# Optimization experiments

Hardware: AMD Instinct MI355X
Metric: run time of the kernel (lower is better)

The kernel has to match this reference:

```python
import jax, jax.numpy as jnp
import numpy as np

NEG = -1e6  # mask fill value used by d2l.sequence_mask


def setup_inputs() -> dict:
    key = jax.random.key(0)
    k1, k2, k3, k4, k5, k6, k7 = jax.random.split(key, 7)
    B, Q, K, DQ, DK, H, DV = 8, 256, 1024, 256, 256, 128, 128
    queries = jax.random.normal(k1, (B, Q, DQ), dtype=jnp.float32)
    keys = jax.random.normal(k2, (B, K, DK), dtype=jnp.float32)
    values = jax.random.normal(k3, (B, K, DV), dtype=jnp.float32)
    valid_lens = jax.random.randint(k4, (B,), 1, K + 1, dtype=jnp.int32)
    # learned params (nn.Linear stores weight as [out, in]; apply as x @ W.T)
    W_q = jax.random.normal(k5, (H, DQ), dtype=jnp.float32) / np.sqrt(DQ)
    W_k = jax.random.normal(k6, (H, DK), dtype=jnp.float32) / np.sqrt(DK)
    w_v = jax.random.normal(k7, (H,), dtype=jnp.float32) / np.sqrt(H)
    return {"queries": queries, "keys": keys, "values": values,
            "valid_lens": valid_lens, "W_q": W_q, "W_k": W_k, "w_v": w_v}


def reference(queries, keys, values, valid_lens, W_q, W_k, w_v):
    # projections
    q = jnp.einsum('bqd,hd->bqh', queries, W_q)   # [B,Q,H]
    k = jnp.einsum('bkd,hd->bkh', keys, W_k)      # [B,K,H]
    # broadcast add + tanh -> [B,Q,K,H] (the fusion-headroom intermediate)
    features = jnp.tanh(q[:, :, None, :] + k[:, None, :, :])
    scores = jnp.einsum('bqkh,h->bqk', features, w_v)  # [B,Q,K]
    # masked softmax: valid_lens is per-batch (dim==1 path)
    klen = scores.shape[-1]
    mask = jnp.arange(klen)[None, None, :] < valid_lens[:, None, None]
    scores = jnp.where(mask, scores, NEG)
    weights = jax.nn.softmax(scores, axis=-1)
    # dropout is identity in eval mode
    return jnp.einsum('bqk,bkv->bqv', weights, values)
```

## Files before the change

kernel.cpp:

```cpp
#include <hip/hip_runtime.h>


#define Bb 8
#define Qn 256
#define Kk 1024
#define Dd 256
#define Hh 128
#define DVv 128

__device__ __forceinline__ float fexp2(float x) { return __builtin_amdgcn_exp2f(x); }
__device__ __forceinline__ float frcp(float x)  { return __builtin_amdgcn_rcpf(x); }

__global__ __launch_bounds__(256)
void repack_w(const float* __restrict__ Wq, const float* __restrict__ Wk,
              float4* __restrict__ Wq4T, float4* __restrict__ Wk4T)
{
    const int blk = blockIdx.x;
    const float* src = (blk < 32) ? Wq : Wk;
    float4*      dst = (blk < 32) ? Wq4T : Wk4T;
    const int idx = (blk & 31) * 256 + threadIdx.x;
    const int g = idx >> 7;
    const int h = idx & 127;
    dst[idx] = *(const float4*)(src + (size_t)h * Dd + g * 4);
}

__global__ __launch_bounds__(512)
void proj_exp_kernel(const float* __restrict__ queries,
                     const float* __restrict__ keys,
                     const float4* __restrict__ Wq4T,
                     const float4* __restrict__ Wk4T,
                     float* __restrict__ EqT,
                     float* __restrict__ EkT)
{
    __shared__ __align__(16) float Xs[16 * 256];
    const int blk = blockIdx.x;
    const float* X; const float4* W4; float* outT; int RB; int i0;
    if (blk < 128) { X = queries; W4 = Wq4T; outT = EqT; RB = Qn; i0 = blk * 16; }
    else           { X = keys;    W4 = Wk4T; outT = EkT; RB = Kk; i0 = (blk - 128) * 16; }
    const int tid = threadIdx.x;
    const int h   = tid & 127;
    const int r4  = __builtin_amdgcn_readfirstlane(tid >> 7);

    {
        const float4* xsrc = (const float4*)(X + (size_t)i0 * Dd);
#pragma unroll
        for (int s = 0; s < 2; ++s) {
            const int idx = tid + 512 * s;
            *(float4*)(Xs + idx * 4) = xsrc[idx];
        }
    }
    __syncthreads();

    float acc[4] = {0.f, 0.f, 0.f, 0.f};
    const float4* wp = W4 + h;
    const float*  xr = Xs + (r4 * 4) * 256;
#pragma unroll 8
    for (int g = 0; g < 64; ++g) {
        const float4 w = wp[(size_t)g * 128];
#pragma unroll
        for (int i = 0; i < 4; ++i) {
            const float4 x = *(const float4*)(xr + i * 256 + g * 4);
            acc[i] = fmaf(x.x, w.x, acc[i]);
            acc[i] = fmaf(x.y, w.y, acc[i]);
            acc[i] = fmaf(x.z, w.z, acc[i]);
            acc[i] = fmaf(x.w, w.w, acc[i]);
        }
    }
    const int b    = i0 / RB;
    const int rloc = (i0 % RB) + r4 * 4;
    float4 o;
    o.x = fexp2(acc[0] * 2.885390082f);
    o.y = fexp2(acc[1] * 2.885390082f);
    o.z = fexp2(acc[2] * 2.885390082f);
    o.w = fexp2(acc[3] * 2.885390082f);
    *(float4*)(outT + (size_t)b * Hh * RB + (size_t)h * RB + rloc) = o;
}

__global__ __launch_bounds__(512)
void score_softmax_pv_kernel(const float* __restrict__ EqT,
                             const float* __restrict__ EkT,
                             const float* __restrict__ wv,
                             const int* __restrict__ valid_lens,
                             const float* __restrict__ values,
                             float* __restrict__ out)
{
    __shared__ __align__(16) float s_sc[4][Kk];
    __shared__ __align__(16) float eqs[Hh * 4];
    __shared__ __align__(16) float w2s[Hh];
    __shared__ float s_inv[4];

    const int blk  = blockIdx.x;
    const int b    = blk & 7;
    const int qt   = blk >> 3;
    const int q0   = qt * 4;
    const int len  = valid_lens[b];
    const int tid  = threadIdx.x;
    const int lane = tid & 63;
    const int wave = __builtin_amdgcn_readfirstlane(tid >> 6);

    if (tid < 128) {
        *(float4*)(eqs + tid * 4) =
            *(const float4*)(EqT + (size_t)b * Hh * Qn + (size_t)tid * Qn + q0);
    } else if (tid < 256) {
        w2s[tid - 128] = -2.0f * wv[tid - 128];
    }
    __syncthreads();

    const float* ekbase = EkT + (size_t)b * Hh * Kk;
#pragma unroll
    for (int kk = 0; kk < 2; ++kk) {
        const int k = tid + kk * 512;
        if ((k & ~63) >= len) continue;
        const float* ekp = ekbase + k;
        float a0 = 0.f, a1 = 0.f, a2 = 0.f, a3 = 0.f;
#pragma unroll 2
        for (int hg = 0; hg < 32; ++hg) {
            const int h = hg << 2;
            const float ek0 = ekp[(size_t)(h + 0) * Kk];
            const float ek1 = ekp[(size_t)(h + 1) * Kk];
            const float ek2 = ekp[(size_t)(h + 2) * Kk];
            const float ek3 = ekp[(size_t)(h + 3) * Kk];
            const float4 w  = *(const float4*)(w2s + h);
            const float4 e0 = *(const float4*)(eqs + (h + 0) * 4);
            const float4 e1 = *(const float4*)(eqs + (h + 1) * 4);
            const float4 e2 = *(const float4*)(eqs + (h + 2) * 4);
            const float4 e3 = *(const float4*)(eqs + (h + 3) * 4);
            {
                const float A = fmaf(e0.x, ek0, 1.0f), B = fmaf(e1.x, ek1, 1.0f);
                const float C = fmaf(e2.x, ek2, 1.0f), E = fmaf(e3.x, ek3, 1.0f);
                const float AB = A * B, CE = C * E;
                const float N = fmaf(fmaf(w.x, B, w.y * A), CE,
                                     fmaf(w.z, E, w.w * C) * AB);
                a0 = fmaf(N, frcp(AB * CE), a0);
            }
            {
                const float A = fmaf(e0.y, ek0, 1.0f), B = fmaf(e1.y, ek1, 1.0f);
                const float C = fmaf(e2.y, ek2, 1.0f), E = fmaf(e3.y, ek3, 1.0f);
                const float AB = A * B, CE = C * E;
                const float N = fmaf(fmaf(w.x, B, w.y * A), CE,
                                     fmaf(w.z, E, w.w * C) * AB);
                a1 = fmaf(N, frcp(AB * CE), a1);
            }
            {
                const float A = fmaf(e0.z, ek0, 1.0f), B = fmaf(e1.z, ek1, 1.0f);
                const float C = fmaf(e2.z, ek2, 1.0f), E = fmaf(e3.z, ek3, 1.0f);
                const float AB = A * B, CE = C * E;
                const float N = fmaf(fmaf(w.x, B, w.y * A), CE,
                                     fmaf(w.z, E, w.w * C) * AB);
                a2 = fmaf(N, frcp(AB * CE), a2);
            }
            {
                const float A = fmaf(e0.w, ek0, 1.0f), B = fmaf(e1.w, ek1, 1.0f);
                const float C = fmaf(e2.w, ek2, 1.0f), E = fmaf(e3.w, ek3, 1.0f);
                const float AB = A * B, CE = C * E;
                const float N = fmaf(fmaf(w.x, B, w.y * A), CE,
                                     fmaf(w.z, E, w.w * C) * AB);
                a3 = fmaf(N, frcp(AB * CE), a3);
            }
        }
        s_sc[0][k] = a0;
        s_sc[1][k] = a1;
        s_sc[2][k] = a2;
        s_sc[3][k] = a3;
    }
    __syncthreads();

    if (wave < 4) {
        const int q = wave;
        float m = -3.0e38f;
        for (int i = lane; i < len; i += 64) m = fmaxf(m, s_sc[q][i]);
#pragma unroll
        for (int off = 32; off > 0; off >>= 1) m = fmaxf(m, __shfl_xor(m, off));
        float sum = 0.f;
        for (int i = lane; i < len; i += 64) {
            const float p = fexp2((s_sc[q][i] - m) * 1.44269504f);
            s_sc[q][i] = p;
            sum += p;
        }
#pragma unroll
        for (int off = 32; off > 0; off >>= 1) sum += __shfl_xor(sum, off);
        if (lane == 0) s_inv[q] = frcp(sum);
    }
    __syncthreads();

    {
        const int slice = tid >> 5;
        const int l32   = tid & 31;
        const int v4    = l32 << 2;
        const float* vp = values + (size_t)b * Kk * DVv + v4;
        float a[4][4];
#pragma unroll
        for (int q = 0; q < 4; ++q) { a[q][0]=0.f; a[q][1]=0.f; a[q][2]=0.f; a[q][3]=0.f; }
        for (int k = slice; k < len; k += 16) {
            const float4 val = *(const float4*)(vp + (size_t)k * DVv);
            const float w0 = s_sc[0][k], w1 = s_sc[1][k], w2 = s_sc[2][k], w3 = s_sc[3][k];
            a[0][0] = fmaf(w0, val.x, a[0][0]);
            a[0][1] = fmaf(w0, val.y, a[0][1]);
            a[0][2] = fmaf(w0, val.z, a[0][2]);
            a[0][3] = fmaf(w0, val.w, a[0][3]);
            a[1][0] = fmaf(w1, val.x, a[1][0]);
            a[1][1] = fmaf(w1, val.y, a[1][1]);
            a[1][2] = fmaf(w1, val.z, a[1][2]);
            a[1][3] = fmaf(w1, val.w, a[1][3]);
            a[2][0] = fmaf(w2, val.x, a[2][0]);
            a[2][1] = fmaf(w2, val.y, a[2][1]);
            a[2][2] = fmaf(w2, val.z, a[2][2]);
            a[2][3] = fmaf(w2, val.w, a[2][3]);
            a[3][0] = fmaf(w3, val.x, a[3][0]);
            a[3][1] = fmaf(w3, val.y, a[3][1]);
            a[3][2] = fmaf(w3, val.z, a[3][2]);
            a[3][3] = fmaf(w3, val.w, a[3][3]);
        }
#pragma unroll
        for (int q = 0; q < 4; ++q)
#pragma unroll
            for (int x = 0; x < 4; ++x) a[q][x] += __shfl_xor(a[q][x], 32);

        __syncthreads();
        float4 (*s_part)[4][32] = (float4 (*)[4][32])(&s_sc[0][0]);
        if (wave > 0 && lane < 32) {
#pragma unroll
            for (int q = 0; q < 4; ++q)
                s_part[wave - 1][q][l32] = make_float4(a[q][0], a[q][1], a[q][2], a[q][3]);
        }
        __syncthreads();
        if (wave == 0 && lane < 32) {
#pragma unroll
            for (int q = 0; q < 4; ++q) {
                float r0 = a[q][0], r1 = a[q][1], r2 = a[q][2], r3 = a[q][3];
#pragma unroll
                for (int w = 0; w < 7; ++w) {
                    const float4 p = s_part[w][q][l32];
                    r0 += p.x; r1 += p.y; r2 += p.z; r3 += p.w;
                }
                const float inv = s_inv[q];
                *(float4*)(out + (size_t)(b * Qn + q0 + q) * DVv + v4) =
                    make_float4(r0 * inv, r1 * inv, r2 * inv, r3 * inv);
            }
        }
    }
}

extern "C" void kernel_launch(void* const* d_in, const int* in_sizes, int n_in,
                              void* d_out, int out_size, void* d_ws, size_t ws_size,
                              hipStream_t stream) {
    (void)in_sizes; (void)n_in; (void)out_size; (void)ws_size;
    const float* queries    = (const float*)d_in[0];
    const float* keys       = (const float*)d_in[1];
    const float* values     = (const float*)d_in[2];
    const int*   valid_lens = (const int*)  d_in[3];
    const float* Wq         = (const float*)d_in[4];
    const float* Wk         = (const float*)d_in[5];
    const float* wvv        = (const float*)d_in[6];
    float* out = (float*)d_out;

    float* Wq4T = (float*)d_ws;
    float* Wk4T = Wq4T + (size_t)Dd * Hh;
    float* EqT  = Wk4T + (size_t)Dd * Hh;
    float* EkT  = EqT + (size_t)Bb * Hh * Qn;

    repack_w       <<<  64, 256, 0, stream>>>(Wq, Wk, (float4*)Wq4T, (float4*)Wk4T);
    proj_exp_kernel<<< 640, 512, 0, stream>>>(queries, keys, (const float4*)Wq4T,
                                              (const float4*)Wk4T, EqT, EkT);
    score_softmax_pv_kernel<<<512, 512, 0, stream>>>(EqT, EkT, wvv, valid_lens,
                                                     values, out);
}
```

Measured before the change: 133.5 us.

## Double threads per block, remap score work to vectorized key loads

The score/softmax/PV kernel now runs with 1024 threads per block. Each thread computes four consecutive keys for a single query, using float4 loads of the transposed key features. The softmax is split across all 16 waves, with the max and sum combined across waves in shared memory. PV accumulation uses 32 slices with a dedicated partial-sum buffer, and batches are swizzled across blocks to balance work under uneven valid lengths. The intent is more parallelism and wider memory loads, at the cost of extra synchronization and register pressure from the stricter launch bounds.

Result: no change. 135.3 us (+1.3%).

```diff
diff --git a/kernel.cpp b/kernel.cpp
--- a/kernel.cpp
+++ b/kernel.cpp
@@ -76,7 +76,7 @@
     *(float4*)(outT + (size_t)b * Hh * RB + (size_t)h * RB + rloc) = o;
 }
 
-__global__ __launch_bounds__(512)
+__global__ __launch_bounds__(1024, 8)
 void score_softmax_pv_kernel(const float* __restrict__ EqT,
                              const float* __restrict__ EkT,
                              const float* __restrict__ wv,
@@ -84,14 +84,16 @@
                              const float* __restrict__ values,
                              float* __restrict__ out)
 {
-    __shared__ __align__(16) float s_sc[4][Kk];
-    __shared__ __align__(16) float eqs[Hh * 4];
-    __shared__ __align__(16) float w2s[Hh];
-    __shared__ float s_inv[4];
+    __shared__ __align__(16) float  s_sc[4][Kk];
+    __shared__ __align__(16) float  eqsT[4][Hh];
+    __shared__ __align__(16) float  w2s[Hh];
+    __shared__ __align__(16) float4 s_part[15][4][32];
+    __shared__ float s_qmax[4][4];
+    __shared__ float s_qsum[4][4];
 
     const int blk  = blockIdx.x;
-    const int b    = blk & 7;
     const int qt   = blk >> 3;
+    const int b    = (blk & 7) ^ ((qt & 32) ? 4 : 0);
     const int q0   = qt * 4;
     const int len  = valid_lens[b];
     const int tid  = threadIdx.x;
@@ -99,87 +101,89 @@
     const int wave = __builtin_amdgcn_readfirstlane(tid >> 6);
 
     if (tid < 128) {
-        *(float4*)(eqs + tid * 4) =
-            *(const float4*)(EqT + (size_t)b * Hh * Qn + (size_t)tid * Qn + q0);
+        const float4 v = *(const float4*)(EqT + (size_t)b * Hh * Qn + (size_t)tid * Qn + q0);
+        eqsT[0][tid] = v.x; eqsT[1][tid] = v.y; eqsT[2][tid] = v.z; eqsT[3][tid] = v.w;
     } else if (tid < 256) {
         w2s[tid - 128] = -2.0f * wv[tid - 128];
     }
     __syncthreads();
 
-    const float* ekbase = EkT + (size_t)b * Hh * Kk;
-#pragma unroll
-    for (int kk = 0; kk < 2; ++kk) {
-        const int k = tid + kk * 512;
-        if ((k & ~63) >= len) continue;
-        const float* ekp = ekbase + k;
+    const int qh = __builtin_amdgcn_readfirstlane(tid >> 8);
+    const int kg = tid & 255;
+    const int kw = ((tid >> 6) & 3) * 256;
+
+    if (kw < len) {
+        const float4* ek4 = (const float4*)(EkT + (size_t)b * Hh * Kk) + kg;
+        const float*  eqv = &eqsT[qh][0];
         float a0 = 0.f, a1 = 0.f, a2 = 0.f, a3 = 0.f;
 #pragma unroll 2
         for (int hg = 0; hg < 32; ++hg) {
             const int h = hg << 2;
-            const float ek0 = ekp[(size_t)(h + 0) * Kk];
-            const float ek1 = ekp[(size_t)(h + 1) * Kk];
-            const float ek2 = ekp[(size_t)(h + 2) * Kk];
-            const float ek3 = ekp[(size_t)(h + 3) * Kk];
-            const float4 w  = *(const float4*)(w2s + h);
-            const float4 e0 = *(const float4*)(eqs + (h + 0) * 4);
-            const float4 e1 = *(const float4*)(eqs + (h + 1) * 4);
-            const float4 e2 = *(const float4*)(eqs + (h + 2) * 4);
-            const float4 e3 = *(const float4*)(eqs + (h + 3) * 4);
-            {
-                const float A = fmaf(e0.x, ek0, 1.0f), B = fmaf(e1.x, ek1, 1.0f);
-                const float C = fmaf(e2.x, ek2, 1.0f), E = fmaf(e3.x, ek3, 1.0f);
-                const float AB = A * B, CE = C * E;
-                const float N = fmaf(fmaf(w.x, B, w.y * A), CE,
-                                     fmaf(w.z, E, w.w * C) * AB);
+            const float4 e0 = ek4[(h + 0) * (Kk / 4)];
+            const float4 e1 = ek4[(h + 1) * (Kk / 4)];
+            const float4 e2 = ek4[(h + 2) * (Kk / 4)];
+            const float4 e3 = ek4[(h + 3) * (Kk / 4)];
+            const float4 q4 = *(const float4*)(eqv + h);
+            const float4 w4 = *(const float4*)(w2s + h);
+            {
+                const float A = fmaf(q4.x, e0.x, 1.f), B = fmaf(q4.y, e1.x, 1.f);
+                const float C = fmaf(q4.z, e2.x, 1.f), E = fmaf(q4.w, e3.x, 1.f);
+                const float AB = A * B, CE = C * E;
+                const float N = fmaf(fmaf(w4.x, B, w4.y * A), CE,
+                                     fmaf(w4.z, E, w4.w * C) * AB);
                 a0 = fmaf(N, frcp(AB * CE), a0);
             }
             {
-                const float A = fmaf(e0.y, ek0, 1.0f), B = fmaf(e1.y, ek1, 1.0f);
-                const float C = fmaf(e2.y, ek2, 1.0f), E = fmaf(e3.y, ek3, 1.0f);
-                const float AB = A * B, CE = C * E;
-                const float N = fmaf(fmaf(w.x, B, w.y * A), CE,
-                                     fmaf(w.z, E, w.w * C) * AB);
+                const float A = fmaf(q4.x, e0.y, 1.f), B = fmaf(q4.y, e1.y, 1.f);
+                const float C = fmaf(q4.z, e2.y, 1.f), E = fmaf(q4.w, e3.y, 1.f);
+                const float AB = A * B, CE = C * E;
+                const float N = fmaf(fmaf(w4.x, B, w4.y * A), CE,
+                                     fmaf(w4.z, E, w4.w * C) * AB);
                 a1 = fmaf(N, frcp(AB * CE), a1);
             }
             {
-                const float A = fmaf(e0.z, ek0, 1.0f), B = fmaf(e1.z, ek1, 1.0f);
-                const float C = fmaf(e2.z, ek2, 1.0f), E = fmaf(e3.z, ek3, 1.0f);
-                const float AB = A * B, CE = C * E;
-                const float N = fmaf(fmaf(w.x, B, w.y * A), CE,
-                                     fmaf(w.z, E, w.w * C) * AB);
+                const float A = fmaf(q4.x, e0.z, 1.f), B = fmaf(q4.y, e1.z, 1.f);
+                const float C = fmaf(q4.z, e2.z, 1.f), E = fmaf(q4.w, e3.z, 1.f);
+                const float AB = A * B, CE = C * E;
+                const float N = fmaf(fmaf(w4.x, B, w4.y * A), CE,
+                                     fmaf(w4.z, E, w4.w * C) * AB);
                 a2 = fmaf(N, frcp(AB * CE), a2);
             }
             {
-                const float A = fmaf(e0.w, ek0, 1.0f), B = fmaf(e1.w, ek1, 1.0f);
-                const float C = fmaf(e2.w, ek2, 1.0f), E = fmaf(e3.w, ek3, 1.0f);
-                const float AB = A * B, CE = C * E;
-                const float N = fmaf(fmaf(w.x, B, w.y * A), CE,
-                                     fmaf(w.z, E, w.w * C) * AB);
+                const float A = fmaf(q4.x, e0.w, 1.f), B = fmaf(q4.y, e1.w, 1.f);
+                const float C = fmaf(q4.z, e2.w, 1.f), E = fmaf(q4.w, e3.w, 1.f);
+                const float AB = A * B, CE = C * E;
+                const float N = fmaf(fmaf(w4.x, B, w4.y * A), CE,
+                                     fmaf(w4.z, E, w4.w * C) * AB);
                 a3 = fmaf(N, frcp(AB * CE), a3);
             }
         }
-        s_sc[0][k] = a0;
-        s_sc[1][k] = a1;
-        s_sc[2][k] = a2;
-        s_sc[3][k] = a3;
-    }
-    __syncthreads();
-
-    if (wave < 4) {
-        const int q = wave;
+        *(float4*)(&s_sc[qh][kg << 2]) = make_float4(a0, a1, a2, a3);
+    }
+    __syncthreads();
+
+    {
+        const int q    = wave & 3;
+        const int qtr  = wave >> 2;
+        const int base = qtr * 256;
+        const int hi   = (base + 256 < len) ? base + 256 : len;
         float m = -3.0e38f;
-        for (int i = lane; i < len; i += 64) m = fmaxf(m, s_sc[q][i]);
+        for (int i = base + lane; i < hi; i += 64) m = fmaxf(m, s_sc[q][i]);
 #pragma unroll
         for (int off = 32; off > 0; off >>= 1) m = fmaxf(m, __shfl_xor(m, off));
+        if (lane == 0) s_qmax[q][qtr] = m;
+        __syncthreads();
+        const float gm = fmaxf(fmaxf(s_qmax[q][0], s_qmax[q][1]),
+                               fmaxf(s_qmax[q][2], s_qmax[q][3]));
         float sum = 0.f;
-        for (int i = lane; i < len; i += 64) {
-            const float p = fexp2((s_sc[q][i] - m) * 1.44269504f);
+        for (int i = base + lane; i < hi; i += 64) {
+            const float p = fexp2((s_sc[q][i] - gm) * 1.44269504f);
             s_sc[q][i] = p;
             sum += p;
         }
 #pragma unroll
         for (int off = 32; off > 0; off >>= 1) sum += __shfl_xor(sum, off);
-        if (lane == 0) s_inv[q] = frcp(sum);
+        if (lane == 0) s_qsum[q][qtr] = sum;
     }
     __syncthreads();
 
@@ -191,7 +195,7 @@
         float a[4][4];
 #pragma unroll
         for (int q = 0; q < 4; ++q) { a[q][0]=0.f; a[q][1]=0.f; a[q][2]=0.f; a[q][3]=0.f; }
-        for (int k = slice; k < len; k += 16) {
+        for (int k = slice; k < len; k += 32) {
             const float4 val = *(const float4*)(vp + (size_t)k * DVv);
             const float w0 = s_sc[0][k], w1 = s_sc[1][k], w2 = s_sc[2][k], w3 = s_sc[3][k];
             a[0][0] = fmaf(w0, val.x, a[0][0]);
@@ -215,9 +219,6 @@
         for (int q = 0; q < 4; ++q)
 #pragma unroll
             for (int x = 0; x < 4; ++x) a[q][x] += __shfl_xor(a[q][x], 32);
-
-        __syncthreads();
-        float4 (*s_part)[4][32] = (float4 (*)[4][32])(&s_sc[0][0]);
         if (wave > 0 && lane < 32) {
 #pragma unroll
             for (int q = 0; q < 4; ++q)
@@ -229,11 +230,12 @@
             for (int q = 0; q < 4; ++q) {
                 float r0 = a[q][0], r1 = a[q][1], r2 = a[q][2], r3 = a[q][3];
 #pragma unroll
-                for (int w = 0; w < 7; ++w) {
+                for (int w = 0; w < 15; ++w) {
                     const float4 p = s_part[w][q][l32];
                     r0 += p.x; r1 += p.y; r2 += p.z; r3 += p.w;
                 }
-                const float inv = s_inv[q];
+                const float inv = frcp(s_qsum[q][0] + s_qsum[q][1] +
+                                       s_qsum[q][2] + s_qsum[q][3]);
                 *(float4*)(out + (size_t)(b * Qn + q0 + q) * DVv + v4) =
                     make_float4(r0 * inv, r1 * inv, r2 * inv, r3 * inv);
             }
@@ -262,6 +264,6 @@
     repack_w       <<<  64, 256, 0, stream>>>(Wq, Wk, (float4*)Wq4T, (float4*)Wk4T);
     proj_exp_kernel<<< 640, 512, 0, stream>>>(queries, keys, (const float4*)Wq4T,
                                               (const float4*)Wk4T, EqT, EkT);
-    score_softmax_pv_kernel<<<512, 512, 0, stream>>>(EqT, EkT, wvv, valid_lens,
-                                                     values, out);
-}
+    score_softmax_pv_kernel<<<512, 1024, 0, stream>>>(EqT, EkT, wvv, valid_lens,
+                                                      values, out);
+}
```
